# Performance work log

Measured on AMD Instinct MI355X. Metric: run time of the kernel, lower is better.

The kernel has to match this reference:

```python
import jax, jax.numpy as jnp
import numpy as np

PS = 32

def _masks(ps):
    yy, xx = np.meshgrid(np.arange(ps), np.arange(ps), indexing='ij')
    c = (ps - 1) / 2.0
    r = np.sqrt((yy - c) ** 2 + (xx - c) ** 2)
    rm = max(r.max(), 1.0)
    ml = (r <= rm / 3.0).astype(np.float32)
    mm = ((r > rm / 3.0) & (r <= 2.0 * rm / 3.0)).astype(np.float32)
    mh = (r > 2.0 * rm / 3.0).astype(np.float32)
    return jnp.asarray(ml), jnp.asarray(mm), jnp.asarray(mh)

MASK_L, MASK_M, MASK_H = _masks(PS)

def setup_inputs() -> dict:
    key = jax.random.key(0)
    ks = jax.random.split(key, 4)
    B, C, H, W = 16, 3, 256, 256
    d = PS * PS            # 1024
    hidden = int(d * 1.5)  # 1536
    c_f = 64
    return {
        'x': jax.random.normal(ks[0], (B, C, H, W), dtype=jnp.float32),
        'W1': jax.random.normal(ks[1], (d, hidden), dtype=jnp.float32) * 0.02,
        'b1': jnp.zeros((hidden,), jnp.float32),
        'W2': jax.random.normal(ks[2], (hidden, d), dtype=jnp.float32) * 0.02,
        'b2': jnp.zeros((d,), jnp.float32),
        'w_proj': jax.random.normal(ks[3], (c_f,), dtype=jnp.float32) * 0.5,
        'gamma': jnp.ones((c_f,), jnp.float32),
        'beta': jnp.zeros((c_f,), jnp.float32),
        'lf_gate': jnp.float32(0.33),
        'mf_gate': jnp.float32(0.34),
        'hf_gate': jnp.float32(0.33),
    }

def _forward(x, W1, b1, W2, b2, w_proj, gamma, beta, lf_gate, mf_gate, hf_gate):
    B, C, H, W = x.shape
    ps = PS
    gh, gw = H // ps, W // ps
    L = gh * gw
    # grayscale
    xg = 0.299 * x[:, 0] + 0.587 * x[:, 1] + 0.114 * x[:, 2]  # [B,H,W]
    # non-overlapping patchify (H,W multiples of ps -> no padding)
    pr = xg.reshape(B, gh, ps, gw, ps).transpose(0, 1, 3, 2, 4).reshape(B, L, ps, ps)
    # per-patch orthonormal FFT2 and magnitude
    mag = jnp.abs(jnp.fft.fft2(pr, norm='ortho'))  # [B,L,ps,ps]
    gate = (jax.nn.sigmoid(lf_gate) * MASK_L
            + jax.nn.sigmoid(mf_gate) * MASK_M
            + jax.nn.sigmoid(hf_gate) * MASK_H)
    mag = mag * gate
    mag_vec = mag.reshape(B * L, ps * ps)
    attn = jax.nn.sigmoid(jax.nn.relu(mag_vec @ W1 + b1) @ W2 + b2)
    mod = mag_vec * attn
    w = mod.mean(axis=-1).reshape(B, L, 1, 1)  # per-patch scalar weight
    recon = pr * (1.0 + w)
    # fold back (exact inverse of the reshape patchify)
    x_rec = recon.reshape(B, gh, gw, ps, ps).transpose(0, 1, 3, 2, 4).reshape(B, H, W)
    # 1x1 conv (1 -> c_f channels, no bias)
    out = x_rec[:, None, :, :] * w_proj[None, :, None, None]  # [B,c_f,H,W]
    # BatchNorm2d (training mode: batch stats, biased variance)
    mean = out.mean(axis=(0, 2, 3), keepdims=True)
    var = out.var(axis=(0, 2, 3), keepdims=True)
    out = (out - mean) * jax.lax.rsqrt(var + 1e-5)
    out = out * gamma[None, :, None, None] + beta[None, :, None, None]
    return jax.nn.relu(out)

def reference(x, W1, b1, W2, b2, w_proj, gamma, beta, lf_gate, mf_gate, hf_gate):
    return _forward(x, W1, b1, W2, b2, w_proj, gamma, beta, lf_gate, mf_gate, hf_gate)
```

## Files before the change

### kernel.cpp

```cpp
#include <hip/hip_runtime.h>
#include <hip/hip_bf16.h>
#include <math.h>

typedef __attribute__((ext_vector_type(8))) short bf16x8;
typedef __attribute__((ext_vector_type(4))) float f32x4;
typedef __attribute__((ext_vector_type(4))) unsigned short u16x4;

static __device__ __forceinline__ float bf2f(unsigned short u) {
    union { unsigned int i; float f; } v; v.i = ((unsigned int)u) << 16; return v.f;
}
static __device__ __forceinline__ unsigned short f2bf(float f) {
    union { float f; unsigned int i; } v; v.f = f;
    unsigned int x = v.i;
    return (unsigned short)((x + 0x7fffu + ((x >> 16) & 1u)) >> 16);
}
static __device__ __forceinline__ float sigmoidf(float v) {
    return 1.0f / (1.0f + expf(-v));
}

__global__ __launch_bounds__(256) void kpatch(
    const float* __restrict__ x, const float* __restrict__ lf,
    const float* __restrict__ mf, const float* __restrict__ hf,
    float* __restrict__ pr_out, unsigned short* __restrict__ mag_bf,
    float* __restrict__ ppsum, float* __restrict__ ppsq)
{
    __shared__ float sX[32][36];
    __shared__ float sYr[32][36];
    __shared__ float sYi[32][36];
    __shared__ float tc[32], ts[32];
    __shared__ float red_s[4], red_q[4];

    const int t = threadIdx.x;
    const int p = blockIdx.x;
    const int b = p >> 6, l = p & 63;
    const int gy = l >> 3, gx = l & 7;
    const int lane = t & 63, wave = t >> 6;

    if (t < 32) {
        float ang = (float)t * 0.19634954084936207f;
        tc[t] = cosf(ang);
        ts[t] = sinf(ang);
    }

    const int y  = t >> 3;
    const int xc = (t & 7) * 4;
    const int h  = gy * 32 + y;
    const int wbase = gx * 32 + xc;
    const long long idx0 = ((long long)(b * 3 + 0) * 256 + h) * 256 + wbase;
    const long long idx1 = ((long long)(b * 3 + 1) * 256 + h) * 256 + wbase;
    const long long idx2 = ((long long)(b * 3 + 2) * 256 + h) * 256 + wbase;
    float4 r4 = *(const float4*)(x + idx0);
    float4 g4 = *(const float4*)(x + idx1);
    float4 b4 = *(const float4*)(x + idx2);
    float4 gray;
    gray.x = 0.299f * r4.x + 0.587f * g4.x + 0.114f * b4.x;
    gray.y = 0.299f * r4.y + 0.587f * g4.y + 0.114f * b4.y;
    gray.z = 0.299f * r4.z + 0.587f * g4.z + 0.114f * b4.z;
    gray.w = 0.299f * r4.w + 0.587f * g4.w + 0.114f * b4.w;
    *(float4*)&sX[y][xc] = gray;
    *(float4*)(pr_out + p * 1024 + t * 4) = gray;

    float ls = gray.x + gray.y + gray.z + gray.w;
    float lq = gray.x * gray.x + gray.y * gray.y + gray.z * gray.z + gray.w * gray.w;
    #pragma unroll
    for (int off = 32; off > 0; off >>= 1) {
        ls += __shfl_down(ls, off, 64);
        lq += __shfl_down(lq, off, 64);
    }
    if (lane == 0) { red_s[wave] = ls; red_q[wave] = lq; }
    __syncthreads();
    if (t == 0) {
        ppsum[p] = red_s[0] + red_s[1] + red_s[2] + red_s[3];
        ppsq[p]  = red_q[0] + red_q[1] + red_q[2] + red_q[3];
    }

    {
        const int k  = t >> 3;
        const int c0 = (t & 7) * 4;
        float yr[4] = {0,0,0,0}, yi[4] = {0,0,0,0};
        for (int n = 0; n < 32; n++) {
            int wi = (k * n) & 31;
            float cw = tc[wi], sw = ts[wi];
            float4 xv = *(const float4*)&sX[n][c0];
            yr[0] += cw * xv.x; yi[0] -= sw * xv.x;
            yr[1] += cw * xv.y; yi[1] -= sw * xv.y;
            yr[2] += cw * xv.z; yi[2] -= sw * xv.z;
            yr[3] += cw * xv.w; yi[3] -= sw * xv.w;
        }
        *(float4*)&sYr[k][c0] = *(float4*)yr;
        *(float4*)&sYi[k][c0] = *(float4*)yi;
    }
    __syncthreads();

    {
        const int k  = t >> 3;
        const int m0 = (t & 7) * 4;
        float zr[4] = {0,0,0,0}, zi[4] = {0,0,0,0};
        for (int c = 0; c < 32; c++) {
            float yr = sYr[k][c];
            float yi = sYi[k][c];
            #pragma unroll
            for (int j = 0; j < 4; j++) {
                int wi = ((m0 + j) * c) & 31;
                float cw = tc[wi], sw = ts[wi];
                zr[j] += yr * cw + yi * sw;
                zi[j] += yi * cw - yr * sw;
            }
        }
        const float sl = sigmoidf(lf[0]);
        const float sm = sigmoidf(mf[0]);
        const float sh = sigmoidf(hf[0]);
        const float T1 = 480.5f / 9.0f;
        const float T2 = 4.0f * 480.5f / 9.0f;
        const float fk = (float)k - 15.5f;
        u16x4 outv;
        #pragma unroll
        for (int j = 0; j < 4; j++) {
            float fm = (float)(m0 + j) - 15.5f;
            float r2 = fk * fk + fm * fm;
            float g = (r2 <= T1) ? sl : ((r2 <= T2) ? sm : sh);
            float magv = sqrtf(zr[j] * zr[j] + zi[j] * zi[j]) * 0.03125f * g;
            outv[j] = f2bf(magv);
        }
        *(u16x4*)(mag_bf + p * 1024 + k * 32 + m0) = outv;
    }
}

__global__ __launch_bounds__(256) void kconv(
    const float* __restrict__ W, unsigned short* __restrict__ WT, int K, int N)
{
    __shared__ float tile[32][33];
    const int k0 = blockIdx.x * 32, n0 = blockIdx.y * 32;
    const int tx = threadIdx.x & 31, ty = threadIdx.x >> 5;
    #pragma unroll
    for (int i = 0; i < 4; i++) {
        int r = ty + i * 8;
        tile[r][tx] = W[(long long)(k0 + r) * N + n0 + tx];
    }
    __syncthreads();
    #pragma unroll
    for (int i = 0; i < 4; i++) {
        int r = ty + i * 8;
        WT[(long long)(n0 + r) * K + k0 + tx] = f2bf(tile[tx][r]);
    }
}

__global__ __launch_bounds__(256) void kgemm1(
    const unsigned short* __restrict__ A, const unsigned short* __restrict__ BT,
    const float* __restrict__ bias, unsigned short* __restrict__ C)
{
    const int K = 1024, N = 1536;
    const int lane = threadIdx.x & 63;
    const int wave = threadIdx.x >> 6;
    const int wm = wave & 1, wn = wave >> 1;
    const int m_base = blockIdx.x * 64 + wm * 32;
    const int n_base = blockIdx.y * 64 + wn * 32;
    const int lr = lane & 15;
    const int koff = (lane >> 4) * 8;

    const unsigned short* pa0 = A  + (long long)(m_base + lr) * K + koff;
    const unsigned short* pa1 = pa0 + (long long)16 * K;
    const unsigned short* pb0 = BT + (long long)(n_base + lr) * K + koff;
    const unsigned short* pb1 = pb0 + (long long)16 * K;

    f32x4 acc00 = {0,0,0,0}, acc01 = {0,0,0,0}, acc10 = {0,0,0,0}, acc11 = {0,0,0,0};

    for (int kk = 0; kk < K; kk += 32) {
        bf16x8 a0 = *(const bf16x8*)(pa0 + kk);
        bf16x8 a1 = *(const bf16x8*)(pa1 + kk);
        bf16x8 b0 = *(const bf16x8*)(pb0 + kk);
        bf16x8 b1 = *(const bf16x8*)(pb1 + kk);
        acc00 = __builtin_amdgcn_mfma_f32_16x16x32_bf16(a0, b0, acc00, 0, 0, 0);
        acc01 = __builtin_amdgcn_mfma_f32_16x16x32_bf16(a0, b1, acc01, 0, 0, 0);
        acc10 = __builtin_amdgcn_mfma_f32_16x16x32_bf16(a1, b0, acc10, 0, 0, 0);
        acc11 = __builtin_amdgcn_mfma_f32_16x16x32_bf16(a1, b1, acc11, 0, 0, 0);
    }

    const int quad = lane >> 4;
    const int col0 = n_base + lr, col1 = col0 + 16;
    const float bias0 = bias[col0], bias1 = bias[col1];
    const int row0b = m_base + quad * 4;
    #pragma unroll
    for (int r = 0; r < 4; r++) {
        int row0 = row0b + r, row1 = row0 + 16;
        C[(long long)row0 * N + col0] = f2bf(fmaxf(acc00[r] + bias0, 0.0f));
        C[(long long)row0 * N + col1] = f2bf(fmaxf(acc01[r] + bias1, 0.0f));
        C[(long long)row1 * N + col0] = f2bf(fmaxf(acc10[r] + bias0, 0.0f));
        C[(long long)row1 * N + col1] = f2bf(fmaxf(acc11[r] + bias1, 0.0f));
    }
}

__global__ __launch_bounds__(256) void kgemm2d(
    const unsigned short* __restrict__ A, const unsigned short* __restrict__ BT,
    const float* __restrict__ bias, const unsigned short* __restrict__ mag,
    float* __restrict__ wpart)
{
    const int K = 1536;
    const int lane = threadIdx.x & 63;
    const int wave = threadIdx.x >> 6;
    const int wm = wave & 1, wn = wave >> 1;
    const int m_base = blockIdx.x * 64 + wm * 32;
    const int n_base = blockIdx.y * 64 + wn * 32;
    const int lr = lane & 15;
    const int koff = (lane >> 4) * 8;

    const unsigned short* pa0 = A  + (long long)(m_base + lr) * K + koff;
    const unsigned short* pa1 = pa0 + (long long)16 * K;
    const unsigned short* pb0 = BT + (long long)(n_base + lr) * K + koff;
    const unsigned short* pb1 = pb0 + (long long)16 * K;

    f32x4 acc00 = {0,0,0,0}, acc01 = {0,0,0,0}, acc10 = {0,0,0,0}, acc11 = {0,0,0,0};

    for (int kk = 0; kk < K; kk += 32) {
        bf16x8 a0 = *(const bf16x8*)(pa0 + kk);
        bf16x8 a1 = *(const bf16x8*)(pa1 + kk);
        bf16x8 b0 = *(const bf16x8*)(pb0 + kk);
        bf16x8 b1 = *(const bf16x8*)(pb1 + kk);
        acc00 = __builtin_amdgcn_mfma_f32_16x16x32_bf16(a0, b0, acc00, 0, 0, 0);
        acc01 = __builtin_amdgcn_mfma_f32_16x16x32_bf16(a0, b1, acc01, 0, 0, 0);
        acc10 = __builtin_amdgcn_mfma_f32_16x16x32_bf16(a1, b0, acc10, 0, 0, 0);
        acc11 = __builtin_amdgcn_mfma_f32_16x16x32_bf16(a1, b1, acc11, 0, 0, 0);
    }

    const int quad = lane >> 4;
    const int col0 = n_base + lr, col1 = col0 + 16;
    const float bias0 = bias[col0], bias1 = bias[col1];
    const int row0b = m_base + quad * 4;

    float dsum0[4], dsum1[4];
    #pragma unroll
    for (int r = 0; r < 4; r++) {
        int row0 = row0b + r, row1 = row0 + 16;
        float v00 = sigmoidf(acc00[r] + bias0);
        float v01 = sigmoidf(acc01[r] + bias1);
        float v10 = sigmoidf(acc10[r] + bias0);
        float v11 = sigmoidf(acc11[r] + bias1);
        float m00 = bf2f(mag[(long long)row0 * 1024 + col0]);
        float m01 = bf2f(mag[(long long)row0 * 1024 + col1]);
        float m10 = bf2f(mag[(long long)row1 * 1024 + col0]);
        float m11 = bf2f(mag[(long long)row1 * 1024 + col1]);
        dsum0[r] = m00 * v00 + m01 * v01;
        dsum1[r] = m10 * v10 + m11 * v11;
    }
    #pragma unroll
    for (int r = 0; r < 4; r++) {
        #pragma unroll
        for (int mask = 8; mask > 0; mask >>= 1) {
            dsum0[r] += __shfl_xor(dsum0[r], mask, 64);
            dsum1[r] += __shfl_xor(dsum1[r], mask, 64);
        }
    }
    if (lr == 0) {
        const int cp = blockIdx.y * 2 + wn;
        #pragma unroll
        for (int r = 0; r < 4; r++) {
            wpart[(row0b + r) * 32 + cp]      = dsum0[r];
            wpart[(row0b + 16 + r) * 32 + cp] = dsum1[r];
        }
    }
}

__global__ __launch_bounds__(1024) void kfin(
    const float* __restrict__ wpart, const float* __restrict__ ppsum,
    const float* __restrict__ ppsq, const float* __restrict__ w_proj,
    const float* __restrict__ gamma, const float* __restrict__ beta,
    float* __restrict__ scales, float* __restrict__ der)
{
    __shared__ float rs[16], rq[16];
    const int p = threadIdx.x;
    const int lane = p & 63, wave = p >> 6;

    const float4* wp4 = (const float4*)(wpart + p * 32);
    float w = 0.0f;
    #pragma unroll
    for (int j = 0; j < 8; j++) {
        float4 v = wp4[j];
        w += v.x + v.y + v.z + v.w;
    }
    float scale = 1.0f + w * (1.0f / 1024.0f);
    scales[p] = scale;

    float s = scale * ppsum[p];
    float q = scale * scale * ppsq[p];
    #pragma unroll
    for (int off = 32; off > 0; off >>= 1) {
        s += __shfl_down(s, off, 64);
        q += __shfl_down(q, off, 64);
    }
    if (lane == 0) { rs[wave] = s; rq[wave] = q; }
    __syncthreads();
    if (p < 64) {
        float S = (p < 16) ? rs[p] : 0.0f;
        float Q = (p < 16) ? rq[p] : 0.0f;
        #pragma unroll
        for (int off = 8; off > 0; off >>= 1) {
            S += __shfl_down(S, off, 64);
            Q += __shfl_down(Q, off, 64);
        }
        S = __shfl(S, 0, 64);
        Q = __shfl(Q, 0, 64);
        const float invN = 1.0f / 1048576.0f;
        float mu  = S * invN;
        float var = Q * invN - mu * mu;
        float wp = w_proj[p];
        float A = wp * gamma[p] / sqrtf(wp * wp * var + 1e-5f);
        der[p]      = A;
        der[64 + p] = beta[p] - A * mu;
    }
}

__global__ __launch_bounds__(256) void kout(
    const float* __restrict__ pr, const float* __restrict__ scales,
    const float* __restrict__ der, float* __restrict__ out)
{
    const int total4 = 16777216;
    for (int i4 = blockIdx.x * 256 + threadIdx.x; i4 < total4; i4 += gridDim.x * 256) {
        const int w4 = i4 & 63;
        const int h = (i4 >> 6) & 255;
        const int plane = i4 >> 14;
        const int c = plane & 63;
        const int b = plane >> 6;
        const int p = (b << 6) + ((h >> 5) << 3) + (w4 >> 3);
        const int off4 = ((h & 31) << 3) + (w4 & 7);
        const float As = der[c] * scales[p];
        const float D2 = der[64 + c];
        float4 v = ((const float4*)pr)[p * 256 + off4];
        float4 o;
        o.x = fmaxf(fmaf(As, v.x, D2), 0.0f);
        o.y = fmaxf(fmaf(As, v.y, D2), 0.0f);
        o.z = fmaxf(fmaf(As, v.z, D2), 0.0f);
        o.w = fmaxf(fmaf(As, v.w, D2), 0.0f);
        ((float4*)out)[i4] = o;
    }
}

extern "C" void kernel_launch(void* const* d_in, const int* in_sizes, int n_in,
                              void* d_out, int out_size, void* d_ws, size_t ws_size,
                              hipStream_t stream)
{
    const float* x      = (const float*)d_in[0];
    const float* W1     = (const float*)d_in[1];
    const float* b1     = (const float*)d_in[2];
    const float* W2     = (const float*)d_in[3];
    const float* b2     = (const float*)d_in[4];
    const float* w_proj = (const float*)d_in[5];
    const float* gamma  = (const float*)d_in[6];
    const float* beta   = (const float*)d_in[7];
    const float* lf     = (const float*)d_in[8];
    const float* mf     = (const float*)d_in[9];
    const float* hf     = (const float*)d_in[10];

    char* ws = (char*)d_ws;
    float* pr                 = (float*)(ws);
    unsigned short* mag_bf    = (unsigned short*)(ws + (4u<<20));
    unsigned short* hidden_bf = (unsigned short*)(ws + (6u<<20));
    unsigned short* w1t       = (unsigned short*)(ws + (10u<<20));
    unsigned short* w2t       = (unsigned short*)(ws + (13u<<20));
    float* wpart              = (float*)(ws + (16u<<20));
    float* ppsum              = (float*)(ws + (17u<<20));
    float* ppsq               = (float*)(ws + (17u<<20) + 4096);
    float* scales             = (float*)(ws + (17u<<20) + 8192);
    float* der                = (float*)(ws + (17u<<20) + 12288);

    kconv<<<dim3(32, 48), 256, 0, stream>>>(W1, w1t, 1024, 1536);
    kconv<<<dim3(48, 32), 256, 0, stream>>>(W2, w2t, 1536, 1024);
    kpatch<<<1024, 256, 0, stream>>>(x, lf, mf, hf, pr, mag_bf, ppsum, ppsq);
    kgemm1<<<dim3(16, 24), 256, 0, stream>>>(mag_bf, w1t, b1, hidden_bf);
    kgemm2d<<<dim3(16, 16), 256, 0, stream>>>(hidden_bf, w2t, b2, mag_bf, wpart);
    kfin<<<1, 1024, 0, stream>>>(wpart, ppsum, ppsq, w_proj, gamma, beta, scales, der);
    kout<<<2048, 256, 0, stream>>>(pr, scales, der, (float*)d_out);
}
```

Measured before the change: 385.0 us.

## Stage GEMM tiles through swizzled LDS, merge weight conversions, nontemporal output stores

```diff
diff --git a/kernel.cpp b/kernel.cpp
--- a/kernel.cpp
+++ b/kernel.cpp
@@ -16,6 +16,11 @@
 }
 static __device__ __forceinline__ float sigmoidf(float v) {
     return 1.0f / (1.0f + expf(-v));
+}
+static __device__ __forceinline__ void gload16(const unsigned short* g, unsigned short* l) {
+    __builtin_amdgcn_global_load_lds(
+        (const __attribute__((address_space(1))) unsigned int*)g,
+        (__attribute__((address_space(3))) unsigned int*)l, 16, 0, 0);
 }
 
 __global__ __launch_bounds__(256) void kpatch(
@@ -126,11 +131,21 @@
     }
 }
 
-__global__ __launch_bounds__(256) void kconv(
-    const float* __restrict__ W, unsigned short* __restrict__ WT, int K, int N)
+__global__ __launch_bounds__(256) void kconvall(
+    const float* __restrict__ W1, const float* __restrict__ W2,
+    unsigned short* __restrict__ w1t, unsigned short* __restrict__ w2t)
 {
     __shared__ float tile[32][33];
-    const int k0 = blockIdx.x * 32, n0 = blockIdx.y * 32;
+    int id = blockIdx.x;
+    const float* W; unsigned short* WT; int K, N, k0, n0;
+    if (id < 1536) {
+        W = W1; WT = w1t; K = 1024; N = 1536;
+        k0 = (id & 31) * 32; n0 = (id >> 5) * 32;
+    } else {
+        id -= 1536;
+        W = W2; WT = w2t; K = 1536; N = 1024;
+        k0 = (id % 48) * 32; n0 = (id / 48) * 32;
+    }
     const int tx = threadIdx.x & 31, ty = threadIdx.x >> 5;
     #pragma unroll
     for (int i = 0; i < 4; i++) {
@@ -150,36 +165,57 @@
     const float* __restrict__ bias, unsigned short* __restrict__ C)
 {
     const int K = 1024, N = 1536;
-    const int lane = threadIdx.x & 63;
-    const int wave = threadIdx.x >> 6;
+    __shared__ unsigned short sA[64 * 64];
+    __shared__ unsigned short sB[64 * 64];
+
+    const int t = threadIdx.x;
+    const int lane = t & 63, wave = t >> 6;
     const int wm = wave & 1, wn = wave >> 1;
-    const int m_base = blockIdx.x * 64 + wm * 32;
-    const int n_base = blockIdx.y * 64 + wn * 32;
-    const int lr = lane & 15;
-    const int koff = (lane >> 4) * 8;
-
-    const unsigned short* pa0 = A  + (long long)(m_base + lr) * K + koff;
-    const unsigned short* pa1 = pa0 + (long long)16 * K;
-    const unsigned short* pb0 = BT + (long long)(n_base + lr) * K + koff;
-    const unsigned short* pb1 = pb0 + (long long)16 * K;
+    const int m0 = blockIdx.x * 64, n0 = blockIdx.y * 64;
+
+    const int u0 = t, u1 = t + 256;
+    const int r0 = u0 >> 3, c0 = (u0 & 7) ^ (r0 & 7);
+    const int r1 = u1 >> 3, c1 = (u1 & 7) ^ (r1 & 7);
+    const unsigned short* agp0 = A  + (long long)(m0 + r0) * K + c0 * 8;
+    const unsigned short* agp1 = A  + (long long)(m0 + r1) * K + c1 * 8;
+    const unsigned short* bgp0 = BT + (long long)(n0 + r0) * K + c0 * 8;
+    const unsigned short* bgp1 = BT + (long long)(n0 + r1) * K + c1 * 8;
+    unsigned short* al0 = sA + u0 * 8;
+    unsigned short* al1 = sA + u1 * 8;
+    unsigned short* bl0 = sB + u0 * 8;
+    unsigned short* bl1 = sB + u1 * 8;
+
+    const int lr = lane & 15, quad = lane >> 4;
+    const int ra0 = wm * 32 + lr, ra1 = ra0 + 16;
+    const int rb0 = wn * 32 + lr, rb1 = rb0 + 16;
+    const int ea = ra0 & 7, eb = rb0 & 7;
 
     f32x4 acc00 = {0,0,0,0}, acc01 = {0,0,0,0}, acc10 = {0,0,0,0}, acc11 = {0,0,0,0};
 
-    for (int kk = 0; kk < K; kk += 32) {
-        bf16x8 a0 = *(const bf16x8*)(pa0 + kk);
-        bf16x8 a1 = *(const bf16x8*)(pa1 + kk);
-        bf16x8 b0 = *(const bf16x8*)(pb0 + kk);
-        bf16x8 b1 = *(const bf16x8*)(pb1 + kk);
-        acc00 = __builtin_amdgcn_mfma_f32_16x16x32_bf16(a0, b0, acc00, 0, 0, 0);
-        acc01 = __builtin_amdgcn_mfma_f32_16x16x32_bf16(a0, b1, acc01, 0, 0, 0);
-        acc10 = __builtin_amdgcn_mfma_f32_16x16x32_bf16(a1, b0, acc10, 0, 0, 0);
-        acc11 = __builtin_amdgcn_mfma_f32_16x16x32_bf16(a1, b1, acc11, 0, 0, 0);
-    }
-
-    const int quad = lane >> 4;
-    const int col0 = n_base + lr, col1 = col0 + 16;
+    for (int kk = 0; kk < K; kk += 64) {
+        __syncthreads();
+        gload16(agp0 + kk, al0);
+        gload16(agp1 + kk, al1);
+        gload16(bgp0 + kk, bl0);
+        gload16(bgp1 + kk, bl1);
+        __syncthreads();
+        #pragma unroll
+        for (int st = 0; st < 2; st++) {
+            const int cq = st * 4 + quad;
+            bf16x8 a0 = *(const bf16x8*)(sA + ra0 * 64 + ((cq ^ ea) << 3));
+            bf16x8 a1 = *(const bf16x8*)(sA + ra1 * 64 + ((cq ^ ea) << 3));
+            bf16x8 b0 = *(const bf16x8*)(sB + rb0 * 64 + ((cq ^ eb) << 3));
+            bf16x8 b1 = *(const bf16x8*)(sB + rb1 * 64 + ((cq ^ eb) << 3));
+            acc00 = __builtin_amdgcn_mfma_f32_16x16x32_bf16(a0, b0, acc00, 0, 0, 0);
+            acc01 = __builtin_amdgcn_mfma_f32_16x16x32_bf16(a0, b1, acc01, 0, 0, 0);
+            acc10 = __builtin_amdgcn_mfma_f32_16x16x32_bf16(a1, b0, acc10, 0, 0, 0);
+            acc11 = __builtin_amdgcn_mfma_f32_16x16x32_bf16(a1, b1, acc11, 0, 0, 0);
+        }
+    }
+
+    const int col0 = n0 + wn * 32 + lr, col1 = col0 + 16;
     const float bias0 = bias[col0], bias1 = bias[col1];
-    const int row0b = m_base + quad * 4;
+    const int row0b = m0 + wm * 32 + quad * 4;
     #pragma unroll
     for (int r = 0; r < 4; r++) {
         int row0 = row0b + r, row1 = row0 + 16;
@@ -196,36 +232,57 @@
     float* __restrict__ wpart)
 {
     const int K = 1536;
-    const int lane = threadIdx.x & 63;
-    const int wave = threadIdx.x >> 6;
+    __shared__ unsigned short sA[64 * 64];
+    __shared__ unsigned short sB[64 * 64];
+
+    const int t = threadIdx.x;
+    const int lane = t & 63, wave = t >> 6;
     const int wm = wave & 1, wn = wave >> 1;
-    const int m_base = blockIdx.x * 64 + wm * 32;
-    const int n_base = blockIdx.y * 64 + wn * 32;
-    const int lr = lane & 15;
-    const int koff = (lane >> 4) * 8;
-
-    const unsigned short* pa0 = A  + (long long)(m_base + lr) * K + koff;
-    const unsigned short* pa1 = pa0 + (long long)16 * K;
-    const unsigned short* pb0 = BT + (long long)(n_base + lr) * K + koff;
-    const unsigned short* pb1 = pb0 + (long long)16 * K;
+    const int m0 = blockIdx.x * 64, n0 = blockIdx.y * 64;
+
+    const int u0 = t, u1 = t + 256;
+    const int r0 = u0 >> 3, c0 = (u0 & 7) ^ (r0 & 7);
+    const int r1 = u1 >> 3, c1 = (u1 & 7) ^ (r1 & 7);
+    const unsigned short* agp0 = A  + (long long)(m0 + r0) * K + c0 * 8;
+    const unsigned short* agp1 = A  + (long long)(m0 + r1) * K + c1 * 8;
+    const unsigned short* bgp0 = BT + (long long)(n0 + r0) * K + c0 * 8;
+    const unsigned short* bgp1 = BT + (long long)(n0 + r1) * K + c1 * 8;
+    unsigned short* al0 = sA + u0 * 8;
+    unsigned short* al1 = sA + u1 * 8;
+    unsigned short* bl0 = sB + u0 * 8;
+    unsigned short* bl1 = sB + u1 * 8;
+
+    const int lr = lane & 15, quad = lane >> 4;
+    const int ra0 = wm * 32 + lr, ra1 = ra0 + 16;
+    const int rb0 = wn * 32 + lr, rb1 = rb0 + 16;
+    const int ea = ra0 & 7, eb = rb0 & 7;
 
     f32x4 acc00 = {0,0,0,0}, acc01 = {0,0,0,0}, acc10 = {0,0,0,0}, acc11 = {0,0,0,0};
 
-    for (int kk = 0; kk < K; kk += 32) {
-        bf16x8 a0 = *(const bf16x8*)(pa0 + kk);
-        bf16x8 a1 = *(const bf16x8*)(pa1 + kk);
-        bf16x8 b0 = *(const bf16x8*)(pb0 + kk);
-        bf16x8 b1 = *(const bf16x8*)(pb1 + kk);
-        acc00 = __builtin_amdgcn_mfma_f32_16x16x32_bf16(a0, b0, acc00, 0, 0, 0);
-        acc01 = __builtin_amdgcn_mfma_f32_16x16x32_bf16(a0, b1, acc01, 0, 0, 0);
-        acc10 = __builtin_amdgcn_mfma_f32_16x16x32_bf16(a1, b0, acc10, 0, 0, 0);
-        acc11 = __builtin_amdgcn_mfma_f32_16x16x32_bf16(a1, b1, acc11, 0, 0, 0);
-    }
-
-    const int quad = lane >> 4;
-    const int col0 = n_base + lr, col1 = col0 + 16;
+    for (int kk = 0; kk < K; kk += 64) {
+        __syncthreads();
+        gload16(agp0 + kk, al0);
+        gload16(agp1 + kk, al1);
+        gload16(bgp0 + kk, bl0);
+        gload16(bgp1 + kk, bl1);
+        __syncthreads();
+        #pragma unroll
+        for (int st = 0; st < 2; st++) {
+            const int cq = st * 4 + quad;
+            bf16x8 a0 = *(const bf16x8*)(sA + ra0 * 64 + ((cq ^ ea) << 3));
+            bf16x8 a1 = *(const bf16x8*)(sA + ra1 * 64 + ((cq ^ ea) << 3));
+            bf16x8 b0 = *(const bf16x8*)(sB + rb0 * 64 + ((cq ^ eb) << 3));
+            bf16x8 b1 = *(const bf16x8*)(sB + rb1 * 64 + ((cq ^ eb) << 3));
+            acc00 = __builtin_amdgcn_mfma_f32_16x16x32_bf16(a0, b0, acc00, 0, 0, 0);
+            acc01 = __builtin_amdgcn_mfma_f32_16x16x32_bf16(a0, b1, acc01, 0, 0, 0);
+            acc10 = __builtin_amdgcn_mfma_f32_16x16x32_bf16(a1, b0, acc10, 0, 0, 0);
+            acc11 = __builtin_amdgcn_mfma_f32_16x16x32_bf16(a1, b1, acc11, 0, 0, 0);
+        }
+    }
+
+    const int col0 = n0 + wn * 32 + lr, col1 = col0 + 16;
     const float bias0 = bias[col0], bias1 = bias[col1];
-    const int row0b = m_base + quad * 4;
+    const int row0b = m0 + wm * 32 + quad * 4;
 
     float dsum0[4], dsum1[4];
     #pragma unroll
@@ -325,12 +382,12 @@
         const float As = der[c] * scales[p];
         const float D2 = der[64 + c];
         float4 v = ((const float4*)pr)[p * 256 + off4];
-        float4 o;
-        o.x = fmaxf(fmaf(As, v.x, D2), 0.0f);
-        o.y = fmaxf(fmaf(As, v.y, D2), 0.0f);
-        o.z = fmaxf(fmaf(As, v.z, D2), 0.0f);
-        o.w = fmaxf(fmaf(As, v.w, D2), 0.0f);
-        ((float4*)out)[i4] = o;
+        f32x4 o;
+        o[0] = fmaxf(fmaf(As, v.x, D2), 0.0f);
+        o[1] = fmaxf(fmaf(As, v.y, D2), 0.0f);
+        o[2] = fmaxf(fmaf(As, v.z, D2), 0.0f);
+        o[3] = fmaxf(fmaf(As, v.w, D2), 0.0f);
+        __builtin_nontemporal_store(o, (f32x4*)out + i4);
     }
 }
 
@@ -362,8 +419,7 @@
     float* scales             = (float*)(ws + (17u<<20) + 8192);
     float* der                = (float*)(ws + (17u<<20) + 12288);
 
-    kconv<<<dim3(32, 48), 256, 0, stream>>>(W1, w1t, 1024, 1536);
-    kconv<<<dim3(48, 32), 256, 0, stream>>>(W2, w2t, 1536, 1024);
+    kconvall<<<3072, 256, 0, stream>>>(W1, W2, w1t, w2t);
     kpatch<<<1024, 256, 0, stream>>>(x, lf, mf, hf, pr, mag_bf, ppsum, ppsq);
     kgemm1<<<dim3(16, 24), 256, 0, stream>>>(mag_bf, w1t, b1, hidden_bf);
     kgemm2d<<<dim3(16, 16), 256, 0, stream>>>(hidden_bf, w2t, b2, mag_bf, wpart);
```

After: 347.8 us. 9.6% less time.
